# Kernel optimization log

Hardware: AMD Instinct MI355X
Metric: run time of the kernel (lower is better)

## Reference

```python
import jax, jax.numpy as jnp
import numpy as np

DIM = 768
HEADS = 8
HEAD_DIM = DIM // HEADS
SCALE = DIM ** (-0.5)  # faithful: original scales by dimension**-0.5, not head_dim


def setup_inputs() -> dict:
    key = jax.random.key(0)
    k1, k2, k3 = jax.random.split(key, 3)
    B, N = 2, 4096
    x = jax.random.normal(k1, (B, N, DIM), dtype=jnp.float32)
    # qkv projection params (Linear(dim, 3*dim))
    W_qkv = jax.random.normal(k2, (DIM, 3 * DIM), dtype=jnp.float32) * (DIM ** -0.5)
    b_qkv = jax.random.normal(k3, (3 * DIM,), dtype=jnp.float32) * 0.01
    return {"x": x, "W_qkv": W_qkv, "b_qkv": b_qkv}


def reference(x, W_qkv, b_qkv):
    B, N, D = x.shape
    qkv = x @ W_qkv + b_qkv                       # (B, N, 3D)
    qkv = qkv.reshape(B, N, 3, HEADS, HEAD_DIM)
    q, k, v = jnp.moveaxis(qkv, 2, 0)             # each (B, N, H, dh)
    # (B, H, N, N) scores — explicit materialization as in the source
    scores = jnp.einsum('bnhd,bmhd->bhnm', q, k) * SCALE
    attn = jax.nn.softmax(scores, axis=-1)
    out = jnp.einsum('bhnm,bmhd->bnhd', attn, v)  # (B, N, H, dh)
    return out.reshape(B, N, D)
```

## Files before the change

### kernel.cpp

```cpp
#include <hip/hip_runtime.h>
#include <hip/hip_bf16.h>


typedef __attribute__((ext_vector_type(8)))  short    bf16x8;
typedef __attribute__((ext_vector_type(4)))  float    floatx4;
typedef __attribute__((ext_vector_type(16))) float    floatx16;
typedef __attribute__((ext_vector_type(8)))  unsigned short us8;
typedef __attribute__((ext_vector_type(4)))  unsigned short us4;

#define HEADS 8
#define DH 96
#define NSEQ 4096
#define DIM 768
#define SCALE2_F (0.03608439182435161f * 1.4426950408889634f)

#define GLOAD16(g, s) __builtin_amdgcn_global_load_lds(                              \
    (const __attribute__((address_space(1))) unsigned int*)(g),                      \
    (__attribute__((address_space(3))) unsigned int*)(s), 16, 0, 0)

__device__ __forceinline__ unsigned short f2bf(float f) {
    union { float f; unsigned u; } v; v.f = f;
    unsigned r = v.u + 0x7fffu + ((v.u >> 16) & 1u);
    return (unsigned short)(r >> 16);
}

__device__ __forceinline__ unsigned pk2(float a, float b) {
    float2 t; t.x = a; t.y = b;
    __hip_bfloat162 r = __float22bfloat162_rn(t);
    return *(unsigned*)&r;
}

__device__ __forceinline__ bf16x8 mk_pfrag(float c0, float c1, float c2, float c3,
                                           float c4, float c5, float c6, float c7, int hB) {
    unsigned pl0 = pk2(c0, c1), pl1 = pk2(c2, c3);
    unsigned pu0 = pk2(c4, c5), pu1 = pk2(c6, c7);
    unsigned s0 = hB ? pl0 : pu0, s1 = hB ? pl1 : pu1;
    unsigned r0 = (unsigned)__shfl_xor((int)s0, 32);
    unsigned r1 = (unsigned)__shfl_xor((int)s1, 32);
    union { unsigned u[4]; bf16x8 v; } f;
    f.u[0] = hB ? r0 : pl0;
    f.u[1] = hB ? r1 : pl1;
    f.u[2] = hB ? pu0 : r0;
    f.u[3] = hB ? pu1 : r1;
    return f.v;
}

__global__ __launch_bounds__(256) void cvt_x(const float* __restrict__ x, unsigned short* __restrict__ xb) {
    int i = blockIdx.x * 256 + threadIdx.x;
    float4 v = ((const float4*)x)[i];
    us4 o; o.x = f2bf(v.x); o.y = f2bf(v.y); o.z = f2bf(v.z); o.w = f2bf(v.w);
    ((us4*)xb)[i] = o;
}

__global__ __launch_bounds__(256) void cvt_w(const float* __restrict__ w, unsigned short* __restrict__ wt) {
    __shared__ unsigned short sm[64][33];
    int c0 = blockIdx.x * 32, k0 = blockIdx.y * 64;
    int t = threadIdx.x;
    int cl = t & 31, kl0 = t >> 5;
    for (int i = 0; i < 8; ++i) {
        int kl = kl0 + i * 8;
        sm[kl][cl] = f2bf(w[(k0 + kl) * 2304 + c0 + cl]);
    }
    __syncthreads();
    int kl2 = t & 63, cl0 = t >> 6;
    for (int i = 0; i < 8; ++i) {
        int cl2 = cl0 + i * 4;
        wt[(c0 + cl2) * 768 + k0 + kl2] = sm[kl2][cl2];
    }
}

__global__ __launch_bounds__(256) void gemm_qk(const unsigned short* __restrict__ xb,
                                               const unsigned short* __restrict__ wt,
                                               const float* __restrict__ bias,
                                               unsigned short* __restrict__ qb,
                                               unsigned short* __restrict__ kb) {
    __shared__ unsigned short As[2][128 * 64];
    __shared__ unsigned short Bs[2][128 * 64];
    const int tid = threadIdx.x;
    const int lane = tid & 63, wv = tid >> 6;
    const int n15 = lane & 15, quad = lane >> 4;
    const int m0 = blockIdx.y * 128, c0 = blockIdx.x * 128;
    const int mw = (wv >> 1) * 64, nw = (wv & 1) * 64;
    const int lrow = lane >> 3, lcol = (lane & 7) * 8;
    floatx4 acc[4][4] = {};

    const unsigned short* ga = xb + (size_t)(m0 + wv * 8 + lrow) * 768 + lcol;
    const unsigned short* gb = wt + (size_t)(c0 + wv * 8 + lrow) * 768 + lcol;
    const int lofs = wv * 8 * 64;

    auto stage = [&](int b, int kt) {
#pragma unroll
        for (int i = 0; i < 4; ++i) {
            GLOAD16(ga + (size_t)i * 32 * 768 + kt * 64, &As[b][lofs + i * 32 * 64]);
            GLOAD16(gb + (size_t)i * 32 * 768 + kt * 64, &Bs[b][lofs + i * 32 * 64]);
        }
    };

    stage(0, 0);
    __syncthreads();
#pragma unroll 2
    for (int kt = 0; kt < 12; ++kt) {
        const int cur = kt & 1;
        if (kt < 11) stage(cur ^ 1, kt + 1);
#pragma unroll
        for (int ks = 0; ks < 2; ++ks) {
            bf16x8 af[4], bfr[4];
            for (int mt = 0; mt < 4; ++mt)
                af[mt] = *(const bf16x8*)&As[cur][(mw + mt * 16 + n15) * 64 + ks * 32 + quad * 8];
            for (int nt = 0; nt < 4; ++nt)
                bfr[nt] = *(const bf16x8*)&Bs[cur][(nw + nt * 16 + n15) * 64 + ks * 32 + quad * 8];
            for (int mt = 0; mt < 4; ++mt)
                for (int nt = 0; nt < 4; ++nt)
                    acc[mt][nt] = __builtin_amdgcn_mfma_f32_16x16x32_bf16(af[mt], bfr[nt], acc[mt][nt], 0, 0, 0);
        }
        __syncthreads();
    }
    for (int nt = 0; nt < 4; ++nt) {
        int c = c0 + nw + nt * 16 + n15;
        float bv = bias[c];
        int which = c / 768, rem = c % 768;
        int h = rem / 96, d = rem % 96;
        for (int mt = 0; mt < 4; ++mt) {
            for (int r = 0; r < 4; ++r) {
                int m = m0 + mw + mt * 16 + quad * 4 + r;
                int b = m >> 12, n = m & 4095;
                float val = acc[mt][nt][r] + bv;
                int bh = b * HEADS + h;
                if (which == 0) qb[(bh * NSEQ + n) * DH + d] = f2bf(val * SCALE2_F);
                else            kb[(bh * NSEQ + n) * DH + d] = f2bf(val);
            }
        }
    }
}

__global__ __launch_bounds__(256) void gemm_v(const unsigned short* __restrict__ xb,
                                              const unsigned short* __restrict__ wt,
                                              const float* __restrict__ bias,
                                              unsigned short* __restrict__ vt) {
    __shared__ unsigned short As[2][128 * 64];
    __shared__ unsigned short Bs[2][128 * 64];
    const int tid = threadIdx.x;
    const int lane = tid & 63, wv = tid >> 6;
    const int n15 = lane & 15, quad = lane >> 4;
    const int m0 = blockIdx.y * 128, c0 = blockIdx.x * 128;
    const int mw = (wv >> 1) * 64, nw = (wv & 1) * 64;
    const int lrow = lane >> 3, lcol = (lane & 7) * 8;
    floatx4 acc[4][4] = {};

    const unsigned short* ga = wt + (size_t)(1536 + m0 + wv * 8 + lrow) * 768 + lcol;
    const unsigned short* gb = xb + (size_t)(c0 + wv * 8 + lrow) * 768 + lcol;
    const int lofs = wv * 8 * 64;

    auto stage = [&](int b, int kt) {
#pragma unroll
        for (int i = 0; i < 4; ++i) {
            GLOAD16(ga + (size_t)i * 32 * 768 + kt * 64, &As[b][lofs + i * 32 * 64]);
            GLOAD16(gb + (size_t)i * 32 * 768 + kt * 64, &Bs[b][lofs + i * 32 * 64]);
        }
    };

    stage(0, 0);
    __syncthreads();
#pragma unroll 2
    for (int kt = 0; kt < 12; ++kt) {
        const int cur = kt & 1;
        if (kt < 11) stage(cur ^ 1, kt + 1);
#pragma unroll
        for (int ks = 0; ks < 2; ++ks) {
            bf16x8 af[4], bfr[4];
            for (int mt = 0; mt < 4; ++mt)
                af[mt] = *(const bf16x8*)&As[cur][(mw + mt * 16 + n15) * 64 + ks * 32 + quad * 8];
            for (int nt = 0; nt < 4; ++nt)
                bfr[nt] = *(const bf16x8*)&Bs[cur][(nw + nt * 16 + n15) * 64 + ks * 32 + quad * 8];
            for (int mt = 0; mt < 4; ++mt)
                for (int nt = 0; nt < 4; ++nt)
                    acc[mt][nt] = __builtin_amdgcn_mfma_f32_16x16x32_bf16(af[mt], bfr[nt], acc[mt][nt], 0, 0, 0);
        }
        __syncthreads();
    }
    for (int mt = 0; mt < 4; ++mt) {
        for (int r = 0; r < 4; ++r) {
            int dv = m0 + mw + mt * 16 + quad * 4 + r;
            float bv = bias[1536 + dv];
            int h = dv / 96, d = dv % 96;
            for (int nt = 0; nt < 4; ++nt) {
                int ng = c0 + nw + nt * 16 + n15;
                int b = ng >> 12, n = ng & 4095;
                vt[((size_t)(b * HEADS + h) * DH + d) * NSEQ + n] = f2bf(acc[mt][nt][r] + bv);
            }
        }
    }
}

__global__ __launch_bounds__(256, 2) void flash(const unsigned short* __restrict__ qb,
                                                const unsigned short* __restrict__ kb,
                                                const unsigned short* __restrict__ vt,
                                                float* __restrict__ out) {
    __shared__ unsigned short sm[34816];
    __shared__ float l_all[128];

    const int tid = threadIdx.x;
    const int lane = tid & 63, wv = tid >> 6;
    const int l31 = lane & 31, h = lane >> 5;
    const int x7 = l31 & 7;
    const int id = blockIdx.x;
    const int bh = id & 15;
    const int q0 = (id >> 4) * 128 + wv * 32;

    const unsigned short* kgb = kb + (size_t)bh * NSEQ * DH;
    const unsigned short* vgb = vt + (size_t)bh * DH * NSEQ;

    bf16x8 qf[6];
    {
        const unsigned short* qrow = qb + (size_t)(bh * NSEQ + q0 + l31) * DH;
#pragma unroll
        for (int ks = 0; ks < 6; ++ks)
            qf[ks] = *(const bf16x8*)&qrow[ks * 16 + h * 8];
    }

    int kofs[2][6];
#pragma unroll
    for (int kt = 0; kt < 2; ++kt)
#pragma unroll
        for (int ks = 0; ks < 6; ++ks) {
            int b = 2 * ks + h;
            int bs = (b < 8) ? (b ^ x7) : (8 + ((b - 8) ^ x7));
            kofs[kt][ks] = (kt * 32 + l31) * 128 + bs * 8;
        }
    int vofs[3][4];
#pragma unroll
    for (int dt = 0; dt < 3; ++dt)
#pragma unroll
        for (int s = 0; s < 4; ++s)
            vofs[dt][s] = (dt * 32 + l31) * 64 + ((2 * s + h) ^ x7) * 8;

    int goffk[3], goffv[3], wofk[3], wofv[3];
#pragma unroll
    for (int i = 0; i < 3; ++i) {
        int tb = i * 256 + tid;
        int r = tb / 12, bb = tb % 12;
        goffk[i] = r * 96 + bb * 8;
        int bs = (bb < 8) ? (bb ^ (r & 7)) : (8 + ((bb - 8) ^ (r & 7)));
        wofk[i] = r * 128 + bs * 8;
        int d = tb >> 3, b2 = tb & 7;
        goffv[i] = d * 4096 + b2 * 8;
        wofv[i] = d * 64 + ((b2 ^ (d & 7))) * 8;
    }

    const floatx16 z16 = (floatx16)(0.f);

    us8 kr[3], vr[3];
    const unsigned short* kpf = kgb;
    const unsigned short* vpf = vgb;
#pragma unroll
    for (int i = 0; i < 3; ++i) { kr[i] = *(const us8*)&kpf[goffk[i]]; vr[i] = *(const us8*)&vpf[goffv[i]]; }
    kpf += 6144; vpf += 64;
#pragma unroll
    for (int i = 0; i < 3; ++i) { *(us8*)&sm[wofk[i]] = kr[i]; *(us8*)&sm[16384 + wofv[i]] = vr[i]; }
#pragma unroll
    for (int i = 0; i < 3; ++i) { kr[i] = *(const us8*)&kpf[goffk[i]]; vr[i] = *(const us8*)&vpf[goffv[i]]; }
    kpf += 6144; vpf += 64;
    __syncthreads();

    floatx16 stA[2], stB[2];
#pragma unroll
    for (int ks = 0; ks < 6; ++ks)
#pragma unroll
        for (int kt = 0; kt < 2; ++kt) {
            bf16x8 ak = *(const bf16x8*)&sm[kofs[kt][ks]];
            stA[kt] = __builtin_amdgcn_mfma_f32_32x32x16_bf16(ak, qf[ks], ks == 0 ? z16 : stA[kt], 0, 0, 0);
        }

    floatx16 o[3] = {};
    float lsum = 0.f;

    auto body = [&](int kv, floatx16 (&cur)[2], floatx16 (&nxt)[2]) {
        if (kv < 63) {
            unsigned short* Kd = sm + ((kv + 1) & 1) * 8192;
            unsigned short* Vd = sm + 16384 + ((kv + 1) % 3) * 6144;
#pragma unroll
            for (int i = 0; i < 3; ++i) { *(us8*)&Kd[wofk[i]] = kr[i]; *(us8*)&Vd[wofv[i]] = vr[i]; }
            if (kv < 62) {
#pragma unroll
                for (int i = 0; i < 3; ++i) { kr[i] = *(const us8*)&kpf[goffk[i]]; vr[i] = *(const us8*)&vpf[goffv[i]]; }
                kpf += 6144; vpf += 64;
            }
        }
        __syncthreads();

        if (kv < 63) {
            const unsigned short* Kn = sm + ((kv + 1) & 1) * 8192;
#pragma unroll
            for (int ks = 0; ks < 6; ++ks)
#pragma unroll
                for (int kt = 0; kt < 2; ++kt) {
                    bf16x8 ak = *(const bf16x8*)&Kn[kofs[kt][ks]];
                    nxt[kt] = __builtin_amdgcn_mfma_f32_32x32x16_bf16(ak, qf[ks], ks == 0 ? z16 : nxt[kt], 0, 0, 0);
                }
        }

#pragma unroll
        for (int kt = 0; kt < 2; ++kt)
#pragma unroll
            for (int rg = 0; rg < 16; ++rg) {
                float p = __builtin_amdgcn_exp2f(cur[kt][rg]);
                cur[kt][rg] = p;
                lsum += p;
            }
        bf16x8 pf[4];
        pf[0] = mk_pfrag(cur[0][0], cur[0][1], cur[0][2], cur[0][3],
                         cur[0][4], cur[0][5], cur[0][6], cur[0][7], h);
        pf[1] = mk_pfrag(cur[0][8], cur[0][9], cur[0][10], cur[0][11],
                         cur[0][12], cur[0][13], cur[0][14], cur[0][15], h);
        pf[2] = mk_pfrag(cur[1][0], cur[1][1], cur[1][2], cur[1][3],
                         cur[1][4], cur[1][5], cur[1][6], cur[1][7], h);
        pf[3] = mk_pfrag(cur[1][8], cur[1][9], cur[1][10], cur[1][11],
                         cur[1][12], cur[1][13], cur[1][14], cur[1][15], h);

        const unsigned short* Vc = sm + 16384 + (kv % 3) * 6144;
#pragma unroll
        for (int s = 0; s < 4; ++s)
#pragma unroll
            for (int dt = 0; dt < 3; ++dt) {
                bf16x8 bv = *(const bf16x8*)&Vc[vofs[dt][s]];
                o[dt] = __builtin_amdgcn_mfma_f32_32x32x16_bf16(pf[s], bv, o[dt], 0, 0, 0);
            }
    };

    for (int kv = 0; kv < 64; kv += 2) {
        body(kv, stA, stB);
        body(kv + 1, stB, stA);
    }

    lsum += __shfl_xor(lsum, 32);
    if (h == 0) l_all[wv * 32 + l31] = lsum;
    __syncthreads();

    const int b = bh >> 3, hd = bh & 7;
#pragma unroll
    for (int rg = 0; rg < 16; ++rg) {
        int row = (rg & 3) + 8 * (rg >> 2) + 4 * h;
        float inv = 1.0f / l_all[wv * 32 + row];
        int q = q0 + row;
        float* op = out + (size_t)(b * NSEQ + q) * DIM + hd * DH;
#pragma unroll
        for (int dt = 0; dt < 3; ++dt)
            op[dt * 32 + l31] = o[dt][rg] * inv;
    }
}

extern "C" void kernel_launch(void* const* d_in, const int* in_sizes, int n_in,
                              void* d_out, int out_size, void* d_ws, size_t ws_size,
                              hipStream_t stream) {
    const float* x    = (const float*)d_in[0];
    const float* W    = (const float*)d_in[1];
    const float* bias = (const float*)d_in[2];
    float* out = (float*)d_out;

    char* ws = (char*)d_ws;
    unsigned short* xb = (unsigned short*)(ws);
    unsigned short* wt = (unsigned short*)(ws + 12582912);
    unsigned short* qb = (unsigned short*)(ws + 16121856);
    unsigned short* kb = (unsigned short*)(ws + 28704768);
    unsigned short* vt = (unsigned short*)(ws + 41287680);

    cvt_x<<<6144, 256, 0, stream>>>(x, xb);
    cvt_w<<<dim3(72, 12), 256, 0, stream>>>(W, wt);
    gemm_qk<<<dim3(12, 64), 256, 0, stream>>>(xb, wt, bias, qb, kb);
    gemm_v<<<dim3(64, 6), 256, 0, stream>>>(xb, wt, bias, vt);
    flash<<<512, 256, 0, stream>>>(qb, kb, vt, out);
}
```

Baseline: 256.7 us.

## Merge QK and V projection GEMMs into one launch with swizzled LDS

Combines the Q/K projection GEMM and the transposed V projection GEMM into a single kernel whose block index selects which path runs, cutting one launch and letting the two tail waves overlap. It also applies an XOR swizzle to the column chunk on both the global-to-LDS staging writes and the LDS fragment reads, to reduce LDS bank conflicts on the row-stride-64 tiles. The branch on block id adds a little divergence-free control overhead and a larger combined grid.

```diff
diff --git a/kernel.cpp b/kernel.cpp
--- a/kernel.cpp
+++ b/kernel.cpp
@@ -69,30 +69,44 @@
     }
 }
 
-__global__ __launch_bounds__(256) void gemm_qk(const unsigned short* __restrict__ xb,
-                                               const unsigned short* __restrict__ wt,
-                                               const float* __restrict__ bias,
-                                               unsigned short* __restrict__ qb,
-                                               unsigned short* __restrict__ kb) {
+__global__ __launch_bounds__(256) void gemm_qkv(const unsigned short* __restrict__ xb,
+                                                const unsigned short* __restrict__ wt,
+                                                const float* __restrict__ bias,
+                                                unsigned short* __restrict__ qb,
+                                                unsigned short* __restrict__ kb,
+                                                unsigned short* __restrict__ vt) {
     __shared__ unsigned short As[2][128 * 64];
     __shared__ unsigned short Bs[2][128 * 64];
     const int tid = threadIdx.x;
     const int lane = tid & 63, wv = tid >> 6;
     const int n15 = lane & 15, quad = lane >> 4;
-    const int m0 = blockIdx.y * 128, c0 = blockIdx.x * 128;
+    const int x7q = n15 & 7;
     const int mw = (wv >> 1) * 64, nw = (wv & 1) * 64;
-    const int lrow = lane >> 3, lcol = (lane & 7) * 8;
+    const int lrow = lane >> 3;
+    const int lcolsw = ((lane & 7) ^ lrow) * 8;
+    const int lofs = wv * 8 * 64;
     floatx4 acc[4][4] = {};
 
-    const unsigned short* ga = xb + (size_t)(m0 + wv * 8 + lrow) * 768 + lcol;
-    const unsigned short* gb = wt + (size_t)(c0 + wv * 8 + lrow) * 768 + lcol;
-    const int lofs = wv * 8 * 64;
+    int id = blockIdx.x;
+    const bool isv = id >= 768;
+    int m0, c0;
+    const unsigned short *gA, *gB;
+    if (!isv) {
+        m0 = (id / 12) * 128; c0 = (id % 12) * 128;
+        gA = xb + (size_t)(m0 + wv * 8 + lrow) * 768 + lcolsw;
+        gB = wt + (size_t)(c0 + wv * 8 + lrow) * 768 + lcolsw;
+    } else {
+        int iv = id - 768;
+        m0 = (iv / 64) * 128; c0 = (iv % 64) * 128;
+        gA = wt + (size_t)(1536 + m0 + wv * 8 + lrow) * 768 + lcolsw;
+        gB = xb + (size_t)(c0 + wv * 8 + lrow) * 768 + lcolsw;
+    }
 
     auto stage = [&](int b, int kt) {
 #pragma unroll
         for (int i = 0; i < 4; ++i) {
-            GLOAD16(ga + (size_t)i * 32 * 768 + kt * 64, &As[b][lofs + i * 32 * 64]);
-            GLOAD16(gb + (size_t)i * 32 * 768 + kt * 64, &Bs[b][lofs + i * 32 * 64]);
+            GLOAD16(gA + (size_t)i * 32 * 768 + kt * 64, &As[b][lofs + i * 32 * 64]);
+            GLOAD16(gB + (size_t)i * 32 * 768 + kt * 64, &Bs[b][lofs + i * 32 * 64]);
         }
     };
 
@@ -106,87 +120,46 @@
         for (int ks = 0; ks < 2; ++ks) {
             bf16x8 af[4], bfr[4];
             for (int mt = 0; mt < 4; ++mt)
-                af[mt] = *(const bf16x8*)&As[cur][(mw + mt * 16 + n15) * 64 + ks * 32 + quad * 8];
+                af[mt] = *(const bf16x8*)&As[cur][(mw + mt * 16 + n15) * 64
+                                                 + (((ks << 2) + quad) ^ x7q) * 8];
             for (int nt = 0; nt < 4; ++nt)
-                bfr[nt] = *(const bf16x8*)&Bs[cur][(nw + nt * 16 + n15) * 64 + ks * 32 + quad * 8];
+                bfr[nt] = *(const bf16x8*)&Bs[cur][(nw + nt * 16 + n15) * 64
+                                                  + (((ks << 2) + quad) ^ x7q) * 8];
             for (int mt = 0; mt < 4; ++mt)
                 for (int nt = 0; nt < 4; ++nt)
                     acc[mt][nt] = __builtin_amdgcn_mfma_f32_16x16x32_bf16(af[mt], bfr[nt], acc[mt][nt], 0, 0, 0);
         }
         __syncthreads();
     }
-    for (int nt = 0; nt < 4; ++nt) {
-        int c = c0 + nw + nt * 16 + n15;
-        float bv = bias[c];
-        int which = c / 768, rem = c % 768;
-        int h = rem / 96, d = rem % 96;
+
+    if (!isv) {
+        for (int nt = 0; nt < 4; ++nt) {
+            int c = c0 + nw + nt * 16 + n15;
+            float bv = bias[c];
+            int which = c / 768, rem = c % 768;
+            int h = rem / 96, d = rem % 96;
+            for (int mt = 0; mt < 4; ++mt) {
+                for (int r = 0; r < 4; ++r) {
+                    int m = m0 + mw + mt * 16 + quad * 4 + r;
+                    int b = m >> 12, n = m & 4095;
+                    float val = acc[mt][nt][r] + bv;
+                    int bh = b * HEADS + h;
+                    if (which == 0) qb[(bh * NSEQ + n) * DH + d] = f2bf(val * SCALE2_F);
+                    else            kb[(bh * NSEQ + n) * DH + d] = f2bf(val);
+                }
+            }
+        }
+    } else {
         for (int mt = 0; mt < 4; ++mt) {
             for (int r = 0; r < 4; ++r) {
-                int m = m0 + mw + mt * 16 + quad * 4 + r;
-                int b = m >> 12, n = m & 4095;
-                float val = acc[mt][nt][r] + bv;
-                int bh = b * HEADS + h;
-                if (which == 0) qb[(bh * NSEQ + n) * DH + d] = f2bf(val * SCALE2_F);
-                else            kb[(bh * NSEQ + n) * DH + d] = f2bf(val);
-            }
-        }
-    }
-}
-
-__global__ __launch_bounds__(256) void gemm_v(const unsigned short* __restrict__ xb,
-                                              const unsigned short* __restrict__ wt,
-                                              const float* __restrict__ bias,
-                                              unsigned short* __restrict__ vt) {
-    __shared__ unsigned short As[2][128 * 64];
-    __shared__ unsigned short Bs[2][128 * 64];
-    const int tid = threadIdx.x;
-    const int lane = tid & 63, wv = tid >> 6;
-    const int n15 = lane & 15, quad = lane >> 4;
-    const int m0 = blockIdx.y * 128, c0 = blockIdx.x * 128;
-    const int mw = (wv >> 1) * 64, nw = (wv & 1) * 64;
-    const int lrow = lane >> 3, lcol = (lane & 7) * 8;
-    floatx4 acc[4][4] = {};
-
-    const unsigned short* ga = wt + (size_t)(1536 + m0 + wv * 8 + lrow) * 768 + lcol;
-    const unsigned short* gb = xb + (size_t)(c0 + wv * 8 + lrow) * 768 + lcol;
-    const int lofs = wv * 8 * 64;
-
-    auto stage = [&](int b, int kt) {
-#pragma unroll
-        for (int i = 0; i < 4; ++i) {
-            GLOAD16(ga + (size_t)i * 32 * 768 + kt * 64, &As[b][lofs + i * 32 * 64]);
-            GLOAD16(gb + (size_t)i * 32 * 768 + kt * 64, &Bs[b][lofs + i * 32 * 64]);
-        }
-    };
-
-    stage(0, 0);
-    __syncthreads();
-#pragma unroll 2
-    for (int kt = 0; kt < 12; ++kt) {
-        const int cur = kt & 1;
-        if (kt < 11) stage(cur ^ 1, kt + 1);
-#pragma unroll
-        for (int ks = 0; ks < 2; ++ks) {
-            bf16x8 af[4], bfr[4];
-            for (int mt = 0; mt < 4; ++mt)
-                af[mt] = *(const bf16x8*)&As[cur][(mw + mt * 16 + n15) * 64 + ks * 32 + quad * 8];
-            for (int nt = 0; nt < 4; ++nt)
-                bfr[nt] = *(const bf16x8*)&Bs[cur][(nw + nt * 16 + n15) * 64 + ks * 32 + quad * 8];
-            for (int mt = 0; mt < 4; ++mt)
-                for (int nt = 0; nt < 4; ++nt)
-                    acc[mt][nt] = __builtin_amdgcn_mfma_f32_16x16x32_bf16(af[mt], bfr[nt], acc[mt][nt], 0, 0, 0);
-        }
-        __syncthreads();
-    }
-    for (int mt = 0; mt < 4; ++mt) {
-        for (int r = 0; r < 4; ++r) {
-            int dv = m0 + mw + mt * 16 + quad * 4 + r;
-            float bv = bias[1536 + dv];
-            int h = dv / 96, d = dv % 96;
-            for (int nt = 0; nt < 4; ++nt) {
-                int ng = c0 + nw + nt * 16 + n15;
-                int b = ng >> 12, n = ng & 4095;
-                vt[((size_t)(b * HEADS + h) * DH + d) * NSEQ + n] = f2bf(acc[mt][nt][r] + bv);
+                int dv = m0 + mw + mt * 16 + quad * 4 + r;
+                float bv = bias[1536 + dv];
+                int h = dv / 96, d = dv % 96;
+                for (int nt = 0; nt < 4; ++nt) {
+                    int ng = c0 + nw + nt * 16 + n15;
+                    int b = ng >> 12, n = ng & 4095;
+                    vt[((size_t)(b * HEADS + h) * DH + d) * NSEQ + n] = f2bf(acc[mt][nt][r] + bv);
+                }
             }
         }
     }
@@ -366,7 +339,6 @@
 
     cvt_x<<<6144, 256, 0, stream>>>(x, xb);
     cvt_w<<<dim3(72, 12), 256, 0, stream>>>(W, wt);
-    gemm_qk<<<dim3(12, 64), 256, 0, stream>>>(xb, wt, bias, qb, kb);
-    gemm_v<<<dim3(64, 6), 256, 0, stream>>>(xb, wt, bias, vt);
+    gemm_qkv<<<1152, 256, 0, stream>>>(xb, wt, bias, qb, kb, vt);
     flash<<<512, 256, 0, stream>>>(qb, kb, vt, out);
 }
```

Result: faster. 250.4 us (-2.5%).
